# Performance work log

Hardware: AMD Instinct MI355X
Metric: run time of the kernel (lower is better)

## Reference

```python
import jax, jax.numpy as jnp
import numpy as np

H_GRU = 32  # GRU hidden size fixed to 32 in the module


def setup_inputs() -> dict:
    key = jax.random.key(0)
    ks = jax.random.split(key, 12)
    B, C_in, H, W = 64, 64, 48, 160
    C_out = 64
    s_in = 1.0 / np.sqrt(C_in)
    s_h = 1.0 / np.sqrt(H_GRU)
    u = lambda k, shape: jax.random.uniform(k, shape, jnp.float32, -s_h, s_h)
    return {
        "x": jax.random.normal(ks[0], (B, C_in, H, W), jnp.float32),
        "conv_w": jax.random.normal(ks[1], (C_out, C_in), jnp.float32) * s_in,
        "conv_b": jax.random.normal(ks[2], (C_out,), jnp.float32) * s_in,
        "wih_f": u(ks[3], (3 * H_GRU, C_out)),
        "whh_f": u(ks[4], (3 * H_GRU, H_GRU)),
        "bih_f": u(ks[5], (3 * H_GRU,)),
        "bhh_f": u(ks[6], (3 * H_GRU,)),
        "wih_b": u(ks[7], (3 * H_GRU, C_out)),
        "whh_b": u(ks[8], (3 * H_GRU, H_GRU)),
        "bih_b": u(ks[9], (3 * H_GRU,)),
        "bhh_b": u(ks[10], (3 * H_GRU,)),
    }


def _gru_scan(pre, whh, bhh):
    # pre: [N, T, 3H] input-side gate pre-activations (already x@Wih^T + bih)
    N = pre.shape[0]

    def step(h, g):
        gh = h @ whh.T + bhh
        gi_r, gi_z, gi_n = jnp.split(g, 3, axis=-1)
        gh_r, gh_z, gh_n = jnp.split(gh, 3, axis=-1)
        r = jax.nn.sigmoid(gi_r + gh_r)
        z = jax.nn.sigmoid(gi_z + gh_z)
        n = jnp.tanh(gi_n + r * gh_n)
        h_new = (1.0 - z) * n + z * h
        return h_new, h_new

    h0 = jnp.zeros((N, H_GRU), pre.dtype)
    _, ys = jax.lax.scan(step, h0, jnp.swapaxes(pre, 0, 1))  # ys: [T, N, H]
    return jnp.swapaxes(ys, 0, 1)  # [N, T, H]


def reference(x, conv_w, conv_b, wih_f, whh_f, bih_f, bhh_f,
              wih_b, whh_b, bih_b, bhh_b):
    B, C_in, H, W = x.shape
    # 1x1 conv fused with the NCHW->NHWC permute
    y = jnp.einsum('bchw,oc->bhwo', x, conv_w) + conv_b  # [B, H, W, C_out]
    C_out = y.shape[-1]
    seq = y.reshape(B * H, W, C_out)  # GRU batch = B*H, seq_len = W
    # forward direction
    pre_f = jnp.einsum('ntc,gc->ntg', seq, wih_f) + bih_f
    out_f = _gru_scan(pre_f, whh_f, bhh_f)
    # backward direction: scan reversed sequence, then flip output back
    seq_r = seq[:, ::-1, :]
    pre_b = jnp.einsum('ntc,gc->ntg', seq_r, wih_b) + bih_b
    out_b = _gru_scan(pre_b, whh_b, bhh_b)[:, ::-1, :]
    out = jnp.concatenate([out_f, out_b], axis=-1)  # [B*H, W, 2*H_GRU]
    out = out.reshape(B, H, W, 2 * H_GRU)
    return jnp.transpose(out, (0, 3, 1, 2))  # back to NCHW
```

## Files before the change

### kernel.cpp

```cpp
#include <hip/hip_runtime.h>


typedef _Float16 f16x8 __attribute__((ext_vector_type(8)));
typedef _Float16 f16x4 __attribute__((ext_vector_type(4)));
typedef __fp16   pk16  __attribute__((ext_vector_type(2)));
typedef float    f32x4 __attribute__((ext_vector_type(4)));

#define HWSTRIDE 7680
#define WS_WHH2_OFF 24576
#define WS_BIAS_OFF 36864
#define WS_X16_OFF  65536
#define NWIN 20

__global__ void fold_weights(const float* __restrict__ conv_w,
                             const float* __restrict__ conv_b,
                             const float* __restrict__ wih_f,
                             const float* __restrict__ bih_f,
                             const float* __restrict__ bhh_f,
                             const float* __restrict__ wih_b,
                             const float* __restrict__ bih_b,
                             const float* __restrict__ bhh_b,
                             const float* __restrict__ whh_f,
                             const float* __restrict__ whh_b,
                             void* wsv)
{
    _Float16* W2   = (_Float16*)wsv;
    _Float16* whh2 = (_Float16*)((char*)wsv + WS_WHH2_OFF);
    float*    bias = (float*)((char*)wsv + WS_BIAS_OFF);
    const int idx = blockIdx.x * 256 + threadIdx.x;
    if (idx < 12288) {
        const int d = idx / 6144, r = idx % 6144, g = r / 64, c = r % 64;
        const float* wih = d ? wih_b : wih_f;
        float acc = 0.f;
        for (int o = 0; o < 64; ++o) acc += wih[g * 64 + o] * conv_w[o * 64 + c];
        W2[idx] = (_Float16)acc;
    } else if (idx < 18432) {
        const int e2 = idx - 12288;
        const int dd = e2 / 3072, rr = e2 % 3072, g = rr / 32, k = rr % 32;
        const int qq = k >> 3, ee = k & 7;
        const int jsrc = (ee < 4) ? (qq * 4 + ee) : (16 + qq * 4 + (ee - 4));
        const float* whh = dd ? whh_b : whh_f;
        whh2[e2] = (_Float16)whh[g * 32 + jsrc];
    } else if (idx < 18688) {
        const int e = idx - 18432;
        const int d = e >> 7, rr = e & 127, kind = rr >> 5, j = rr & 31;
        const float* wih = d ? wih_b : wih_f;
        const float* bih = d ? bih_b : bih_f;
        const float* bhh = d ? bhh_b : bhh_f;
        float v;
        if (kind == 0 || kind == 1) {
            const int g = j + kind * 32;
            float b2 = bih[g];
            for (int o = 0; o < 64; ++o) b2 += wih[g * 64 + o] * conv_b[o];
            v = b2 + bhh[g];
        } else if (kind == 2) {
            const int g = j + 64;
            float b2 = bih[g];
            for (int o = 0; o < 64; ++o) b2 += wih[g * 64 + o] * conv_b[o];
            v = b2;
        } else {
            v = bhh[j + 64];
        }
        bias[(d * 4 + kind) * 32 + j] = v;
    }
}

static __device__ __forceinline__ unsigned pkh(float a, float b) {
    pk16 p = __builtin_amdgcn_cvt_pkrtz(a, b);
    return __builtin_bit_cast(unsigned, p);
}

__global__ __launch_bounds__(256, 2)
void xpose(const float* __restrict__ x, _Float16* __restrict__ x16)
{
    __shared__ _Float16 tile[16 * 16 * 64];
    const int bid = blockIdx.x;
    const int wc  = bid % 10;
    const int hg  = (bid / 10) % 3;
    const int b   = bid / 30;
    const int t   = threadIdx.x;
    const int s   = t >> 4;
    const int c2  = t & 15;
    const float* xb = x + (size_t)b * 64 * HWSTRIDE + (size_t)(hg * 16) * 160 + wc * 16;

    float4 pf[4][4];
    #pragma unroll
    for (int cc = 0; cc < 4; ++cc)
        #pragma unroll
        for (int k = 0; k < 4; ++k)
            pf[cc][k] = *(const float4*)(xb + (size_t)(c2 * 4 + cc) * HWSTRIDE
                                         + (size_t)s * 160 + k * 4);
    #pragma unroll
    for (int k = 0; k < 4; ++k)
        #pragma unroll
        for (int m = 0; m < 4; ++m) {
            const int w = k * 4 + m;
            uint2 v;
            v.x = pkh(((const float*)&pf[0][k])[m], ((const float*)&pf[1][k])[m]);
            v.y = pkh(((const float*)&pf[2][k])[m], ((const float*)&pf[3][k])[m]);
            const int baddr = (s * 2048 + w * 128 + c2 * 8) ^ ((s & 7) << 4);
            *(uint2*)((char*)tile + baddr) = v;
        }
    __syncthreads();
    #pragma unroll
    for (int k = 0; k < 4; ++k) {
        const int w  = k * 4 + (t >> 6);
        const int ss = (t & 63) >> 2;
        const int c0 = (t & 3) * 16;
        uint2 dv[4];
        #pragma unroll
        for (int j = 0; j < 4; ++j) {
            const int baddr = (ss * 2048 + w * 128 + c0 * 2 + j * 8) ^ ((ss & 7) << 4);
            dv[j] = *(const uint2*)((char*)tile + baddr);
        }
        _Float16* op = x16 + ((size_t)(b * 3 + hg) * 160 + wc * 16 + w) * 1024 + ss * 64 + c0;
        *(uint4*)(op)     = make_uint4(dv[0].x, dv[0].y, dv[1].x, dv[1].y);
        *(uint4*)(op + 8) = make_uint4(dv[2].x, dv[2].y, dv[3].x, dv[3].y);
    }
}

__global__ __launch_bounds__(64, 1)
void gru_fused9(const _Float16* __restrict__ x16,
                const void* __restrict__ wsv,
                float* __restrict__ out)
{
    const int bid   = blockIdx.x;
    const int d     = bid & 1;
    const int slice = bid >> 1;
    const int b     = slice / 3;
    const int hg    = slice % 3;
    const int h0    = hg * 16;
    const int lane  = threadIdx.x;
    const int q     = lane >> 4;
    const int s16   = lane & 15;

    const _Float16* W2 = (const _Float16*)wsv + (size_t)d * 96 * 64;
    f16x8 W2A[6][2];
    #pragma unroll
    for (int gt = 0; gt < 6; ++gt)
        #pragma unroll
        for (int kt = 0; kt < 2; ++kt)
            W2A[gt][kt] = *(const f16x8*)&W2[(gt * 16 + s16) * 64 + kt * 32 + q * 8];
    const _Float16* whh2 = (const _Float16*)((const char*)wsv + WS_WHH2_OFF)
                           + (size_t)d * 96 * 32;
    f16x8 whhA[6];
    #pragma unroll
    for (int gt = 0; gt < 6; ++gt)
        whhA[gt] = *(const f16x8*)&whh2[(gt * 16 + s16) * 32 + q * 8];
    const float* bias = (const float*)((const char*)wsv + WS_BIAS_OFF) + d * 128;
    float biasC[6][4];
    #pragma unroll
    for (int gt = 0; gt < 6; ++gt)
        #pragma unroll
        for (int r = 0; r < 4; ++r)
            biasC[gt][r] = bias[(gt >> 1) * 32 + (gt & 1) * 16 + 4 * q + r];
    float bhN[2][4];
    #pragma unroll
    for (int jh = 0; jh < 2; ++jh)
        #pragma unroll
        for (int r = 0; r < 4; ++r)
            bhN[jh][r] = bias[96 + jh * 16 + 4 * q + r];

    const _Float16* xsl = x16 + (size_t)slice * 160 * 1024 + s16 * 64 + q * 8;
    float* ob = out + ((size_t)b * 64 + d * 32) * HWSTRIDE + (size_t)(h0 + s16) * 160;

    f16x8 B0r[4], B1r[4];
    auto loadB = [&](int s, f16x8& B0d, f16x8& B1d) {
        const _Float16* p = xsl + (size_t)(d ? (159 - s) : s) * 1024;
        B0d = *(const f16x8*)(p);
        B1d = *(const f16x8*)(p + 32);
    };
    #pragma unroll
    for (int s0 = 0; s0 < 4; ++s0) loadB(s0, B0r[s0], B1r[s0]);

    f16x8 hB = {};
    f16x8 hB8[8];
    float hprev[8];
    #pragma unroll
    for (int uu = 0; uu < 8; ++uu) hprev[uu] = 0.f;

    #pragma unroll 1
    for (int i = 0; i < NWIN; ++i) {
        #pragma unroll
        for (int tt = 0; tt < 8; ++tt) {
            const int s = i * 8 + tt;
            f32x4 aR0 = {biasC[0][0], biasC[0][1], biasC[0][2], biasC[0][3]};
            f32x4 aR1 = {biasC[1][0], biasC[1][1], biasC[1][2], biasC[1][3]};
            f32x4 aZ0 = {biasC[2][0], biasC[2][1], biasC[2][2], biasC[2][3]};
            f32x4 aZ1 = {biasC[3][0], biasC[3][1], biasC[3][2], biasC[3][3]};
            f32x4 pN0 = {biasC[4][0], biasC[4][1], biasC[4][2], biasC[4][3]};
            f32x4 pN1 = {biasC[5][0], biasC[5][1], biasC[5][2], biasC[5][3]};
            f32x4 hN0 = {bhN[0][0], bhN[0][1], bhN[0][2], bhN[0][3]};
            f32x4 hN1 = {bhN[1][0], bhN[1][1], bhN[1][2], bhN[1][3]};
            aR0 = __builtin_amdgcn_mfma_f32_16x16x32_f16(W2A[0][0], B0r[tt & 3], aR0, 0, 0, 0);
            aR0 = __builtin_amdgcn_mfma_f32_16x16x32_f16(W2A[0][1], B1r[tt & 3], aR0, 0, 0, 0);
            aR1 = __builtin_amdgcn_mfma_f32_16x16x32_f16(W2A[1][0], B0r[tt & 3], aR1, 0, 0, 0);
            aR1 = __builtin_amdgcn_mfma_f32_16x16x32_f16(W2A[1][1], B1r[tt & 3], aR1, 0, 0, 0);
            aZ0 = __builtin_amdgcn_mfma_f32_16x16x32_f16(W2A[2][0], B0r[tt & 3], aZ0, 0, 0, 0);
            aZ0 = __builtin_amdgcn_mfma_f32_16x16x32_f16(W2A[2][1], B1r[tt & 3], aZ0, 0, 0, 0);
            aZ1 = __builtin_amdgcn_mfma_f32_16x16x32_f16(W2A[3][0], B0r[tt & 3], aZ1, 0, 0, 0);
            aZ1 = __builtin_amdgcn_mfma_f32_16x16x32_f16(W2A[3][1], B1r[tt & 3], aZ1, 0, 0, 0);
            pN0 = __builtin_amdgcn_mfma_f32_16x16x32_f16(W2A[4][0], B0r[tt & 3], pN0, 0, 0, 0);
            pN0 = __builtin_amdgcn_mfma_f32_16x16x32_f16(W2A[4][1], B1r[tt & 3], pN0, 0, 0, 0);
            pN1 = __builtin_amdgcn_mfma_f32_16x16x32_f16(W2A[5][0], B0r[tt & 3], pN1, 0, 0, 0);
            pN1 = __builtin_amdgcn_mfma_f32_16x16x32_f16(W2A[5][1], B1r[tt & 3], pN1, 0, 0, 0);
            aR0 = __builtin_amdgcn_mfma_f32_16x16x32_f16(whhA[0], hB, aR0, 0, 0, 0);
            aR1 = __builtin_amdgcn_mfma_f32_16x16x32_f16(whhA[1], hB, aR1, 0, 0, 0);
            aZ0 = __builtin_amdgcn_mfma_f32_16x16x32_f16(whhA[2], hB, aZ0, 0, 0, 0);
            aZ1 = __builtin_amdgcn_mfma_f32_16x16x32_f16(whhA[3], hB, aZ1, 0, 0, 0);
            hN0 = __builtin_amdgcn_mfma_f32_16x16x32_f16(whhA[4], hB, hN0, 0, 0, 0);
            hN1 = __builtin_amdgcn_mfma_f32_16x16x32_f16(whhA[5], hB, hN1, 0, 0, 0);
            if (tt < 4) {
                loadB(s + 4, B0r[tt & 3], B1r[tt & 3]);
            } else if (i + 1 < NWIN) {
                loadB(s + 4, B0r[tt & 3], B1r[tt & 3]);
            }
            float hn[8];
            #pragma unroll
            for (int r = 0; r < 4; ++r) {
                const float rr = __builtin_amdgcn_rcpf(1.f + __expf(-aR0[r]));
                const float zz = __builtin_amdgcn_rcpf(1.f + __expf(-aZ0[r]));
                float ta = fmaf(rr, hN0[r], pN0[r]);
                ta = fminf(fmaxf(ta, -15.f), 15.f);
                const float e2 = __expf(2.f * ta);
                const float nn = (e2 - 1.f) * __builtin_amdgcn_rcpf(e2 + 1.f);
                hn[r] = (1.f - zz) * nn + zz * hprev[r];
            }
            #pragma unroll
            for (int r = 0; r < 4; ++r) {
                const float rr = __builtin_amdgcn_rcpf(1.f + __expf(-aR1[r]));
                const float zz = __builtin_amdgcn_rcpf(1.f + __expf(-aZ1[r]));
                float ta = fmaf(rr, hN1[r], pN1[r]);
                ta = fminf(fmaxf(ta, -15.f), 15.f);
                const float e2 = __expf(2.f * ta);
                const float nn = (e2 - 1.f) * __builtin_amdgcn_rcpf(e2 + 1.f);
                hn[4 + r] = (1.f - zz) * nn + zz * hprev[4 + r];
            }
            {
                uint4 hu;
                hu.x = pkh(hn[0], hn[1]); hu.y = pkh(hn[2], hn[3]);
                hu.z = pkh(hn[4], hn[5]); hu.w = pkh(hn[6], hn[7]);
                hB = __builtin_bit_cast(f16x8, hu);
            }
            hB8[tt] = hB;
            #pragma unroll
            for (int uu = 0; uu < 8; ++uu) hprev[uu] = hn[uu];
        }
        {
            const int w0 = d ? (152 - 8 * i) : (8 * i);
            #pragma unroll
            for (int e = 0; e < 8; ++e) {
                const int j = (e >> 2) * 16 + 4 * q + (e & 3);
                float* pw = ob + (size_t)j * HWSTRIDE + w0;
                if (d == 0) {
                    *(float4*)(pw)     = make_float4((float)hB8[0][e], (float)hB8[1][e],
                                                     (float)hB8[2][e], (float)hB8[3][e]);
                    *(float4*)(pw + 4) = make_float4((float)hB8[4][e], (float)hB8[5][e],
                                                     (float)hB8[6][e], (float)hB8[7][e]);
                } else {
                    *(float4*)(pw)     = make_float4((float)hB8[7][e], (float)hB8[6][e],
                                                     (float)hB8[5][e], (float)hB8[4][e]);
                    *(float4*)(pw + 4) = make_float4((float)hB8[3][e], (float)hB8[2][e],
                                                     (float)hB8[1][e], (float)hB8[0][e]);
                }
            }
        }
    }
}

#define BAR() do { asm volatile("s_waitcnt lgkmcnt(0)" ::: "memory"); \
                   __builtin_amdgcn_s_barrier();                      \
                   asm volatile("" ::: "memory"); } while (0)

__global__ __launch_bounds__(128, 1)
void gru_fused8(const float* __restrict__ x,
                const void* __restrict__ wsv,
                float* __restrict__ out)
{
    __shared__ __align__(16) _Float16 xt[1024 * 8];
    __shared__ __align__(16) _Float16 spre[2 * 8 * 16 * 96];

    const int bid  = blockIdx.x;
    const int d    = bid / 192;
    const int g    = bid % 192;
    const int b    = g / 3;
    const int h0   = (g % 3) * 16;
    const int lane = threadIdx.x & 63;
    const int wave = threadIdx.x >> 6;
    const int sw   = bid & 1;
    const int q    = lane >> 4;
    const int s16  = lane & 15;

    const float* xb = x + (size_t)b * 64 * HWSTRIDE + (size_t)h0 * 160;

    if (wave != sw) {
        const _Float16* W2 = (const _Float16*)wsv + (size_t)d * 96 * 64;
        f16x8 W2A[6][2];
        #pragma unroll
        for (int gt = 0; gt < 6; ++gt)
            #pragma unroll
            for (int kt = 0; kt < 2; ++kt)
                W2A[gt][kt] = *(const f16x8*)&W2[(gt * 16 + s16) * 64 + kt * 32 + q * 8];
        const float* bias = (const float*)((const char*)wsv + WS_BIAS_OFF) + d * 128;
        float biasC[6][4];
        #pragma unroll
        for (int gt = 0; gt < 6; ++gt)
            #pragma unroll
            for (int r = 0; r < 4; ++r)
                biasC[gt][r] = bias[(gt >> 1) * 32 + (gt & 1) * 16 + 4 * q + r];

        float4 pf[32];
        auto load_win = [&](int wi) {
            const int w0 = d ? (152 - 8 * wi) : (8 * wi);
            #pragma unroll
            for (int k = 0; k < 16; ++k) {
                const int row = lane + 64 * k;
                const float* p = xb + (size_t)(row >> 4) * HWSTRIDE + (row & 15) * 160 + w0;
                pf[2 * k]     = *(const float4*)p;
                pf[2 * k + 1] = *(const float4*)(p + 4);
            }
        };
        auto write_xt = [&]() {
            #pragma unroll
            for (int k = 0; k < 16; ++k) {
                const int row = lane + 64 * k;
                uint4 v;
                v.x = pkh(pf[2*k].x,   pf[2*k].y);
                v.y = pkh(pf[2*k].z,   pf[2*k].w);
                v.z = pkh(pf[2*k+1].x, pf[2*k+1].y);
                v.w = pkh(pf[2*k+1].z, pf[2*k+1].w);
                *(uint4*)&xt[row * 8] = v;
            }
        };
        auto project = [&](int wi) {
            _Float16* sp = &spre[(wi & 1) * 12288];
            for (int tt = 0; tt < 8; ++tt) {
                const int wl = d ? (7 - tt) : tt;
                const int base0 = (q * 8) * 128 + s16 * 8 + wl;
                f16x8 B0, B1;
                #pragma unroll
                for (int e = 0; e < 8; ++e) {
                    B0[e] = xt[base0 + e * 128];
                    B1[e] = xt[base0 + e * 128 + 4096];
                }
                #pragma unroll
                for (int gt = 0; gt < 6; ++gt) {
                    f32x4 acc = {biasC[gt][0], biasC[gt][1], biasC[gt][2], biasC[gt][3]};
                    acc = __builtin_amdgcn_mfma_f32_16x16x32_f16(W2A[gt][0], B0, acc, 0, 0, 0);
                    acc = __builtin_amdgcn_mfma_f32_16x16x32_f16(W2A[gt][1], B1, acc, 0, 0, 0);
                    uint2 v; v.x = pkh(acc[0], acc[1]); v.y = pkh(acc[2], acc[3]);
                    const int col = (gt * 16 + 4 * q) ^ ((s16 & 7) << 2);
                    *(uint2*)&sp[(tt * 16 + s16) * 96 + col] = v;
                }
            }
        };

        load_win(0);
        #pragma unroll 1
        for (int i = 0; i < NWIN; ++i) {
            write_xt();
            project(i);
            if (i + 1 < NWIN) load_win(i + 1);
            BAR();
        }
    } else {
        const _Float16* whh2 = (const _Float16*)((const char*)wsv + WS_WHH2_OFF)
                               + (size_t)d * 96 * 32;
        f16x8 whhA[6];
        #pragma unroll
        for (int gt = 0; gt < 6; ++gt)
            whhA[gt] = *(const f16x8*)&whh2[(gt * 16 + s16) * 32 + q * 8];
        const float* bias = (const float*)((const char*)wsv + WS_BIAS_OFF) + d * 128;
        float bhN[2][4];
        #pragma unroll
        for (int jh = 0; jh < 2; ++jh)
            #pragma unroll
            for (int r = 0; r < 4; ++r)
                bhN[jh][r] = bias[96 + jh * 16 + 4 * q + r];

        float* ob = out + ((size_t)b * 64 + d * 32) * HWSTRIDE + (size_t)(h0 + s16) * 160;
        f16x8 hB = {};
        f16x8 hB8[8];
        float hprev[8];
        #pragma unroll
        for (int uu = 0; uu < 8; ++uu) hprev[uu] = 0.f;

        int spcol[6];
        #pragma unroll
        for (int gt = 0; gt < 6; ++gt)
            spcol[gt] = (gt * 16 + 4 * q) ^ ((s16 & 7) << 2);

        #pragma unroll 1
        for (int i = 0; i < NWIN; ++i) {
            BAR();
            const _Float16* sp = &spre[(i & 1) * 12288];
            f16x4 pg[4][6];
            #pragma unroll
            for (int tt = 0; tt < 8; ++tt) {
                if ((tt & 3) == 0) {
                    #pragma unroll
                    for (int t4 = 0; t4 < 4; ++t4)
                        #pragma unroll
                        for (int gt = 0; gt < 6; ++gt)
                            pg[t4][gt] = *(const f16x4*)
                                &sp[((tt + t4) * 16 + s16) * 96 + spcol[gt]];
                }
                const f16x4 p0 = pg[tt & 3][0], p1 = pg[tt & 3][1];
                const f16x4 p2 = pg[tt & 3][2], p3 = pg[tt & 3][3];
                const f16x4 p4 = pg[tt & 3][4], p5 = pg[tt & 3][5];
                f32x4 aR0 = {(float)p0[0], (float)p0[1], (float)p0[2], (float)p0[3]};
                f32x4 aR1 = {(float)p1[0], (float)p1[1], (float)p1[2], (float)p1[3]};
                f32x4 aZ0 = {(float)p2[0], (float)p2[1], (float)p2[2], (float)p2[3]};
                f32x4 aZ1 = {(float)p3[0], (float)p3[1], (float)p3[2], (float)p3[3]};
                f32x4 aN0 = {bhN[0][0], bhN[0][1], bhN[0][2], bhN[0][3]};
                f32x4 aN1 = {bhN[1][0], bhN[1][1], bhN[1][2], bhN[1][3]};
                aR0 = __builtin_amdgcn_mfma_f32_16x16x32_f16(whhA[0], hB, aR0, 0, 0, 0);
                aR1 = __builtin_amdgcn_mfma_f32_16x16x32_f16(whhA[1], hB, aR1, 0, 0, 0);
                aZ0 = __builtin_amdgcn_mfma_f32_16x16x32_f16(whhA[2], hB, aZ0, 0, 0, 0);
                aZ1 = __builtin_amdgcn_mfma_f32_16x16x32_f16(whhA[3], hB, aZ1, 0, 0, 0);
                aN0 = __builtin_amdgcn_mfma_f32_16x16x32_f16(whhA[4], hB, aN0, 0, 0, 0);
                aN1 = __builtin_amdgcn_mfma_f32_16x16x32_f16(whhA[5], hB, aN1, 0, 0, 0);
                float hn[8];
                #pragma unroll
                for (int r = 0; r < 4; ++r) {
                    const float rr = __builtin_amdgcn_rcpf(1.f + __expf(-aR0[r]));
                    const float zz = __builtin_amdgcn_rcpf(1.f + __expf(-aZ0[r]));
                    float ta = fmaf(rr, aN0[r], (float)p4[r]);
                    ta = fminf(fmaxf(ta, -15.f), 15.f);
                    const float e2 = __expf(2.f * ta);
                    const float nn = (e2 - 1.f) * __builtin_amdgcn_rcpf(e2 + 1.f);
                    hn[r] = (1.f - zz) * nn + zz * hprev[r];
                }
                #pragma unroll
                for (int r = 0; r < 4; ++r) {
                    const float rr = __builtin_amdgcn_rcpf(1.f + __expf(-aR1[r]));
                    const float zz = __builtin_amdgcn_rcpf(1.f + __expf(-aZ1[r]));
                    float ta = fmaf(rr, aN1[r], (float)p5[r]);
                    ta = fminf(fmaxf(ta, -15.f), 15.f);
                    const float e2 = __expf(2.f * ta);
                    const float nn = (e2 - 1.f) * __builtin_amdgcn_rcpf(e2 + 1.f);
                    hn[4 + r] = (1.f - zz) * nn + zz * hprev[4 + r];
                }
                {
                    uint4 hu;
                    hu.x = pkh(hn[0], hn[1]); hu.y = pkh(hn[2], hn[3]);
                    hu.z = pkh(hn[4], hn[5]); hu.w = pkh(hn[6], hn[7]);
                    hB = __builtin_bit_cast(f16x8, hu);
                }
                hB8[tt] = hB;
                #pragma unroll
                for (int uu = 0; uu < 8; ++uu) hprev[uu] = hn[uu];
            }
            {
                const int w0 = d ? (152 - 8 * i) : (8 * i);
                #pragma unroll
                for (int e = 0; e < 8; ++e) {
                    const int j = (e >> 2) * 16 + 4 * q + (e & 3);
                    float* pw = ob + (size_t)j * HWSTRIDE + w0;
                    if (d == 0) {
                        *(float4*)(pw) = make_float4((float)hB8[0][e], (float)hB8[1][e],
                                                     (float)hB8[2][e], (float)hB8[3][e]);
                        *(float4*)(pw + 4) = make_float4((float)hB8[4][e], (float)hB8[5][e],
                                                         (float)hB8[6][e], (float)hB8[7][e]);
                    } else {
                        *(float4*)(pw) = make_float4((float)hB8[7][e], (float)hB8[6][e],
                                                     (float)hB8[5][e], (float)hB8[4][e]);
                        *(float4*)(pw + 4) = make_float4((float)hB8[3][e], (float)hB8[2][e],
                                                         (float)hB8[1][e], (float)hB8[0][e]);
                    }
                }
            }
        }
    }
}

extern "C" void kernel_launch(void* const* d_in, const int* in_sizes, int n_in,
                              void* d_out, int out_size, void* d_ws, size_t ws_size,
                              hipStream_t stream) {
    (void)in_sizes; (void)n_in; (void)out_size;
    fold_weights<<<dim3(74), dim3(256), 0, stream>>>(
        (const float*)d_in[1],
        (const float*)d_in[2],
        (const float*)d_in[3],
        (const float*)d_in[5],
        (const float*)d_in[6],
        (const float*)d_in[7],
        (const float*)d_in[9],
        (const float*)d_in[10],
        (const float*)d_in[4],
        (const float*)d_in[8],
        d_ws);
    const size_t need = (size_t)WS_X16_OFF + (size_t)192 * 160 * 1024 * 2;
    if (ws_size >= need) {
        _Float16* x16 = (_Float16*)((char*)d_ws + WS_X16_OFF);
        xpose<<<dim3(1920), dim3(256), 0, stream>>>((const float*)d_in[0], x16);
        gru_fused9<<<dim3(384), dim3(64), 0, stream>>>(x16, d_ws, (float*)d_out);
    } else {
        gru_fused8<<<dim3(384), dim3(128), 0, stream>>>(
            (const float*)d_in[0], d_ws, (float*)d_out);
    }
}
```

Measured before the change: 204.6 us.

## Interleave two independent GRU slices per wavefront to hide recurrence latency

The GRU kernel now processes two H-slices per single-wave block, alternating their recurrent steps. While one step's MFMA and transcendental chain is in flight, the other slice's independent work can issue, which hides latency inside the serial recurrence. The grid shrinks from 384 to 192 blocks, so fewer CUs are busy, and each block's serial chain becomes twice as long. Loads are double-buffered with a two-step prefetch, output is written every four steps, and xpose splits its prefetch into halves so it can run at higher occupancy.

```diff
diff --git a/kernel.cpp b/kernel.cpp
--- a/kernel.cpp
+++ b/kernel.cpp
@@ -10,7 +10,6 @@
 #define WS_WHH2_OFF 24576
 #define WS_BIAS_OFF 36864
 #define WS_X16_OFF  65536
-#define NWIN 20
 
 __global__ void fold_weights(const float* __restrict__ conv_w,
                              const float* __restrict__ conv_b,
@@ -70,7 +69,7 @@
     return __builtin_bit_cast(unsigned, p);
 }
 
-__global__ __launch_bounds__(256, 2)
+__global__ __launch_bounds__(256, 4)
 void xpose(const float* __restrict__ x, _Float16* __restrict__ x16)
 {
     __shared__ _Float16 tile[16 * 16 * 64];
@@ -83,24 +82,27 @@
     const int c2  = t & 15;
     const float* xb = x + (size_t)b * 64 * HWSTRIDE + (size_t)(hg * 16) * 160 + wc * 16;
 
-    float4 pf[4][4];
     #pragma unroll
-    for (int cc = 0; cc < 4; ++cc)
-        #pragma unroll
-        for (int k = 0; k < 4; ++k)
-            pf[cc][k] = *(const float4*)(xb + (size_t)(c2 * 4 + cc) * HWSTRIDE
-                                         + (size_t)s * 160 + k * 4);
-    #pragma unroll
-    for (int k = 0; k < 4; ++k)
-        #pragma unroll
-        for (int m = 0; m < 4; ++m) {
-            const int w = k * 4 + m;
-            uint2 v;
-            v.x = pkh(((const float*)&pf[0][k])[m], ((const float*)&pf[1][k])[m]);
-            v.y = pkh(((const float*)&pf[2][k])[m], ((const float*)&pf[3][k])[m]);
-            const int baddr = (s * 2048 + w * 128 + c2 * 8) ^ ((s & 7) << 4);
-            *(uint2*)((char*)tile + baddr) = v;
-        }
+    for (int half = 0; half < 2; ++half) {
+        float4 pf[4][2];
+        #pragma unroll
+        for (int cc = 0; cc < 4; ++cc)
+            #pragma unroll
+            for (int k = 0; k < 2; ++k)
+                pf[cc][k] = *(const float4*)(xb + (size_t)(c2 * 4 + cc) * HWSTRIDE
+                                             + (size_t)s * 160 + (half * 2 + k) * 4);
+        #pragma unroll
+        for (int k = 0; k < 2; ++k)
+            #pragma unroll
+            for (int m = 0; m < 4; ++m) {
+                const int w = (half * 2 + k) * 4 + m;
+                uint2 v;
+                v.x = pkh(((const float*)&pf[0][k])[m], ((const float*)&pf[1][k])[m]);
+                v.y = pkh(((const float*)&pf[2][k])[m], ((const float*)&pf[3][k])[m]);
+                const int baddr = (s * 2048 + w * 128 + c2 * 8) ^ ((s & 7) << 4);
+                *(uint2*)((char*)tile + baddr) = v;
+            }
+    }
     __syncthreads();
     #pragma unroll
     for (int k = 0; k < 4; ++k) {
@@ -120,19 +122,16 @@
 }
 
 __global__ __launch_bounds__(64, 1)
-void gru_fused9(const _Float16* __restrict__ x16,
-                const void* __restrict__ wsv,
-                float* __restrict__ out)
+void gru_fused10(const _Float16* __restrict__ x16,
+                 const void* __restrict__ wsv,
+                 float* __restrict__ out)
 {
-    const int bid   = blockIdx.x;
-    const int d     = bid & 1;
-    const int slice = bid >> 1;
-    const int b     = slice / 3;
-    const int hg    = slice % 3;
-    const int h0    = hg * 16;
-    const int lane  = threadIdx.x;
-    const int q     = lane >> 4;
-    const int s16   = lane & 15;
+    const int bid  = blockIdx.x;
+    const int d    = bid & 1;
+    const int pr   = bid >> 1;
+    const int lane = threadIdx.x;
+    const int q    = lane >> 4;
+    const int s16  = lane & 15;
 
     const _Float16* W2 = (const _Float16*)wsv + (size_t)d * 96 * 64;
     f16x8 W2A[6][2];
@@ -161,108 +160,117 @@
         for (int r = 0; r < 4; ++r)
             bhN[jh][r] = bias[96 + jh * 16 + 4 * q + r];
 
-    const _Float16* xsl = x16 + (size_t)slice * 160 * 1024 + s16 * 64 + q * 8;
-    float* ob = out + ((size_t)b * 64 + d * 32) * HWSTRIDE + (size_t)(h0 + s16) * 160;
-
-    f16x8 B0r[4], B1r[4];
-    auto loadB = [&](int s, f16x8& B0d, f16x8& B1d) {
-        const _Float16* p = xsl + (size_t)(d ? (159 - s) : s) * 1024;
-        B0d = *(const f16x8*)(p);
-        B1d = *(const f16x8*)(p + 32);
+    const int slA = pr * 2, slB = pr * 2 + 1;
+    const _Float16* xsA = x16 + (size_t)slA * 160 * 1024 + s16 * 64 + q * 8;
+    const _Float16* xsB = x16 + (size_t)slB * 160 * 1024 + s16 * 64 + q * 8;
+    float* obA = out + ((size_t)(slA / 3) * 64 + d * 32) * HWSTRIDE
+               + (size_t)((slA % 3) * 16 + s16) * 160;
+    float* obB = out + ((size_t)(slB / 3) * 64 + d * 32) * HWSTRIDE
+               + (size_t)((slB % 3) * 16 + s16) * 160;
+
+    f16x8 rA0[2], rA1[2], rB0[2], rB1[2];
+    auto ldA = [&](int s, int slot) {
+        const _Float16* p = xsA + (size_t)(d ? (159 - s) : s) * 1024;
+        rA0[slot] = *(const f16x8*)(p);
+        rA1[slot] = *(const f16x8*)(p + 32);
     };
-    #pragma unroll
-    for (int s0 = 0; s0 < 4; ++s0) loadB(s0, B0r[s0], B1r[s0]);
-
-    f16x8 hB = {};
-    f16x8 hB8[8];
-    float hprev[8];
-    #pragma unroll
-    for (int uu = 0; uu < 8; ++uu) hprev[uu] = 0.f;
+    auto ldB = [&](int s, int slot) {
+        const _Float16* p = xsB + (size_t)(d ? (159 - s) : s) * 1024;
+        rB0[slot] = *(const f16x8*)(p);
+        rB1[slot] = *(const f16x8*)(p + 32);
+    };
+    ldA(0, 0); ldB(0, 0);
+    ldA(1, 1); ldB(1, 1);
+
+    f16x8 hA = {}, hBc = {};
+    f16x8 sbA[4], sbB[4];
+
+    auto gru_step = [&](const f16x8 B0c, const f16x8 B1c, f16x8& hc) {
+        f32x4 aR0 = {biasC[0][0], biasC[0][1], biasC[0][2], biasC[0][3]};
+        f32x4 aR1 = {biasC[1][0], biasC[1][1], biasC[1][2], biasC[1][3]};
+        f32x4 aZ0 = {biasC[2][0], biasC[2][1], biasC[2][2], biasC[2][3]};
+        f32x4 aZ1 = {biasC[3][0], biasC[3][1], biasC[3][2], biasC[3][3]};
+        f32x4 pN0 = {biasC[4][0], biasC[4][1], biasC[4][2], biasC[4][3]};
+        f32x4 pN1 = {biasC[5][0], biasC[5][1], biasC[5][2], biasC[5][3]};
+        f32x4 hN0 = {bhN[0][0], bhN[0][1], bhN[0][2], bhN[0][3]};
+        f32x4 hN1 = {bhN[1][0], bhN[1][1], bhN[1][2], bhN[1][3]};
+        aR0 = __builtin_amdgcn_mfma_f32_16x16x32_f16(W2A[0][0], B0c, aR0, 0, 0, 0);
+        aR0 = __builtin_amdgcn_mfma_f32_16x16x32_f16(W2A[0][1], B1c, aR0, 0, 0, 0);
+        aR1 = __builtin_amdgcn_mfma_f32_16x16x32_f16(W2A[1][0], B0c, aR1, 0, 0, 0);
+        aR1 = __builtin_amdgcn_mfma_f32_16x16x32_f16(W2A[1][1], B1c, aR1, 0, 0, 0);
+        aZ0 = __builtin_amdgcn_mfma_f32_16x16x32_f16(W2A[2][0], B0c, aZ0, 0, 0, 0);
+        aZ0 = __builtin_amdgcn_mfma_f32_16x16x32_f16(W2A[2][1], B1c, aZ0, 0, 0, 0);
+        aZ1 = __builtin_amdgcn_mfma_f32_16x16x32_f16(W2A[3][0], B0c, aZ1, 0, 0, 0);
+        aZ1 = __builtin_amdgcn_mfma_f32_16x16x32_f16(W2A[3][1], B1c, aZ1, 0, 0, 0);
+        pN0 = __builtin_amdgcn_mfma_f32_16x16x32_f16(W2A[4][0], B0c, pN0, 0, 0, 0);
+        pN0 = __builtin_amdgcn_mfma_f32_16x16x32_f16(W2A[4][1], B1c, pN0, 0, 0, 0);
+        pN1 = __builtin_amdgcn_mfma_f32_16x16x32_f16(W2A[5][0], B0c, pN1, 0, 0, 0);
+        pN1 = __builtin_amdgcn_mfma_f32_16x16x32_f16(W2A[5][1], B1c, pN1, 0, 0, 0);
+        aR0 = __builtin_amdgcn_mfma_f32_16x16x32_f16(whhA[0], hc, aR0, 0, 0, 0);
+        aR1 = __builtin_amdgcn_mfma_f32_16x16x32_f16(whhA[1], hc, aR1, 0, 0, 0);
+        aZ0 = __builtin_amdgcn_mfma_f32_16x16x32_f16(whhA[2], hc, aZ0, 0, 0, 0);
+        aZ1 = __builtin_amdgcn_mfma_f32_16x16x32_f16(whhA[3], hc, aZ1, 0, 0, 0);
+        hN0 = __builtin_amdgcn_mfma_f32_16x16x32_f16(whhA[4], hc, hN0, 0, 0, 0);
+        hN1 = __builtin_amdgcn_mfma_f32_16x16x32_f16(whhA[5], hc, hN1, 0, 0, 0);
+        float hn[8];
+        #pragma unroll
+        for (int r = 0; r < 4; ++r) {
+            const float rr = __builtin_amdgcn_rcpf(1.f + __expf(-aR0[r]));
+            const float zz = __builtin_amdgcn_rcpf(1.f + __expf(-aZ0[r]));
+            float ta = fmaf(rr, hN0[r], pN0[r]);
+            ta = fminf(fmaxf(ta, -15.f), 15.f);
+            const float e2 = __expf(2.f * ta);
+            const float nn = (e2 - 1.f) * __builtin_amdgcn_rcpf(e2 + 1.f);
+            hn[r] = fmaf(zz, (float)hc[r] - nn, nn);
+        }
+        #pragma unroll
+        for (int r = 0; r < 4; ++r) {
+            const float rr = __builtin_amdgcn_rcpf(1.f + __expf(-aR1[r]));
+            const float zz = __builtin_amdgcn_rcpf(1.f + __expf(-aZ1[r]));
+            float ta = fmaf(rr, hN1[r], pN1[r]);
+            ta = fminf(fmaxf(ta, -15.f), 15.f);
+            const float e2 = __expf(2.f * ta);
+            const float nn = (e2 - 1.f) * __builtin_amdgcn_rcpf(e2 + 1.f);
+            hn[4 + r] = fmaf(zz, (float)hc[4 + r] - nn, nn);
+        }
+        uint4 hu;
+        hu.x = pkh(hn[0], hn[1]); hu.y = pkh(hn[2], hn[3]);
+        hu.z = pkh(hn[4], hn[5]); hu.w = pkh(hn[6], hn[7]);
+        hc = __builtin_bit_cast(f16x8, hu);
+    };
 
     #pragma unroll 1
-    for (int i = 0; i < NWIN; ++i) {
-        #pragma unroll
-        for (int tt = 0; tt < 8; ++tt) {
-            const int s = i * 8 + tt;
-            f32x4 aR0 = {biasC[0][0], biasC[0][1], biasC[0][2], biasC[0][3]};
-            f32x4 aR1 = {biasC[1][0], biasC[1][1], biasC[1][2], biasC[1][3]};
-            f32x4 aZ0 = {biasC[2][0], biasC[2][1], biasC[2][2], biasC[2][3]};
-            f32x4 aZ1 = {biasC[3][0], biasC[3][1], biasC[3][2], biasC[3][3]};
-            f32x4 pN0 = {biasC[4][0], biasC[4][1], biasC[4][2], biasC[4][3]};
-            f32x4 pN1 = {biasC[5][0], biasC[5][1], biasC[5][2], biasC[5][3]};
-            f32x4 hN0 = {bhN[0][0], bhN[0][1], bhN[0][2], bhN[0][3]};
-            f32x4 hN1 = {bhN[1][0], bhN[1][1], bhN[1][2], bhN[1][3]};
-            aR0 = __builtin_amdgcn_mfma_f32_16x16x32_f16(W2A[0][0], B0r[tt & 3], aR0, 0, 0, 0);
-            aR0 = __builtin_amdgcn_mfma_f32_16x16x32_f16(W2A[0][1], B1r[tt & 3], aR0, 0, 0, 0);
-            aR1 = __builtin_amdgcn_mfma_f32_16x16x32_f16(W2A[1][0], B0r[tt & 3], aR1, 0, 0, 0);
-            aR1 = __builtin_amdgcn_mfma_f32_16x16x32_f16(W2A[1][1], B1r[tt & 3], aR1, 0, 0, 0);
-            aZ0 = __builtin_amdgcn_mfma_f32_16x16x32_f16(W2A[2][0], B0r[tt & 3], aZ0, 0, 0, 0);
-            aZ0 = __builtin_amdgcn_mfma_f32_16x16x32_f16(W2A[2][1], B1r[tt & 3], aZ0, 0, 0, 0);
-            aZ1 = __builtin_amdgcn_mfma_f32_16x16x32_f16(W2A[3][0], B0r[tt & 3], aZ1, 0, 0, 0);
-            aZ1 = __builtin_amdgcn_mfma_f32_16x16x32_f16(W2A[3][1], B1r[tt & 3], aZ1, 0, 0, 0);
-            pN0 = __builtin_amdgcn_mfma_f32_16x16x32_f16(W2A[4][0], B0r[tt & 3], pN0, 0, 0, 0);
-            pN0 = __builtin_amdgcn_mfma_f32_16x16x32_f16(W2A[4][1], B1r[tt & 3], pN0, 0, 0, 0);
-            pN1 = __builtin_amdgcn_mfma_f32_16x16x32_f16(W2A[5][0], B0r[tt & 3], pN1, 0, 0, 0);
-            pN1 = __builtin_amdgcn_mfma_f32_16x16x32_f16(W2A[5][1], B1r[tt & 3], pN1, 0, 0, 0);
-            aR0 = __builtin_amdgcn_mfma_f32_16x16x32_f16(whhA[0], hB, aR0, 0, 0, 0);
-            aR1 = __builtin_amdgcn_mfma_f32_16x16x32_f16(whhA[1], hB, aR1, 0, 0, 0);
-            aZ0 = __builtin_amdgcn_mfma_f32_16x16x32_f16(whhA[2], hB, aZ0, 0, 0, 0);
-            aZ1 = __builtin_amdgcn_mfma_f32_16x16x32_f16(whhA[3], hB, aZ1, 0, 0, 0);
-            hN0 = __builtin_amdgcn_mfma_f32_16x16x32_f16(whhA[4], hB, hN0, 0, 0, 0);
-            hN1 = __builtin_amdgcn_mfma_f32_16x16x32_f16(whhA[5], hB, hN1, 0, 0, 0);
-            if (tt < 4) {
-                loadB(s + 4, B0r[tt & 3], B1r[tt & 3]);
-            } else if (i + 1 < NWIN) {
-                loadB(s + 4, B0r[tt & 3], B1r[tt & 3]);
-            }
-            float hn[8];
-            #pragma unroll
-            for (int r = 0; r < 4; ++r) {
-                const float rr = __builtin_amdgcn_rcpf(1.f + __expf(-aR0[r]));
-                const float zz = __builtin_amdgcn_rcpf(1.f + __expf(-aZ0[r]));
-                float ta = fmaf(rr, hN0[r], pN0[r]);
-                ta = fminf(fmaxf(ta, -15.f), 15.f);
-                const float e2 = __expf(2.f * ta);
-                const float nn = (e2 - 1.f) * __builtin_amdgcn_rcpf(e2 + 1.f);
-                hn[r] = (1.f - zz) * nn + zz * hprev[r];
-            }
-            #pragma unroll
-            for (int r = 0; r < 4; ++r) {
-                const float rr = __builtin_amdgcn_rcpf(1.f + __expf(-aR1[r]));
-                const float zz = __builtin_amdgcn_rcpf(1.f + __expf(-aZ1[r]));
-                float ta = fmaf(rr, hN1[r], pN1[r]);
-                ta = fminf(fmaxf(ta, -15.f), 15.f);
-                const float e2 = __expf(2.f * ta);
-                const float nn = (e2 - 1.f) * __builtin_amdgcn_rcpf(e2 + 1.f);
-                hn[4 + r] = (1.f - zz) * nn + zz * hprev[4 + r];
-            }
-            {
-                uint4 hu;
-                hu.x = pkh(hn[0], hn[1]); hu.y = pkh(hn[2], hn[3]);
-                hu.z = pkh(hn[4], hn[5]); hu.w = pkh(hn[6], hn[7]);
-                hB = __builtin_bit_cast(f16x8, hu);
-            }
-            hB8[tt] = hB;
-            #pragma unroll
-            for (int uu = 0; uu < 8; ++uu) hprev[uu] = hn[uu];
-        }
-        {
-            const int w0 = d ? (152 - 8 * i) : (8 * i);
-            #pragma unroll
-            for (int e = 0; e < 8; ++e) {
-                const int j = (e >> 2) * 16 + 4 * q + (e & 3);
-                float* pw = ob + (size_t)j * HWSTRIDE + w0;
-                if (d == 0) {
-                    *(float4*)(pw)     = make_float4((float)hB8[0][e], (float)hB8[1][e],
-                                                     (float)hB8[2][e], (float)hB8[3][e]);
-                    *(float4*)(pw + 4) = make_float4((float)hB8[4][e], (float)hB8[5][e],
-                                                     (float)hB8[6][e], (float)hB8[7][e]);
-                } else {
-                    *(float4*)(pw)     = make_float4((float)hB8[7][e], (float)hB8[6][e],
-                                                     (float)hB8[5][e], (float)hB8[4][e]);
-                    *(float4*)(pw + 4) = make_float4((float)hB8[3][e], (float)hB8[2][e],
-                                                     (float)hB8[1][e], (float)hB8[0][e]);
-                }
+    for (int i = 0; i < 40; ++i) {
+        #pragma unroll
+        for (int tt = 0; tt < 4; ++tt) {
+            const int s = i * 4 + tt;
+            const int slot = s & 1;
+            const f16x8 a0 = rA0[slot], a1 = rA1[slot];
+            const f16x8 b0 = rB0[slot], b1 = rB1[slot];
+            int s2 = s + 2; if (s2 > 159) s2 = 159;
+            ldA(s2, slot);
+            ldB(s2, slot);
+            gru_step(a0, a1, hA);
+            sbA[tt] = hA;
+            gru_step(b0, b1, hBc);
+            sbB[tt] = hBc;
+        }
+        const int w0 = d ? (156 - 4 * i) : (4 * i);
+        #pragma unroll
+        for (int e = 0; e < 8; ++e) {
+            const int j = (e >> 2) * 16 + 4 * q + (e & 3);
+            float* pwA = obA + (size_t)j * HWSTRIDE + w0;
+            float* pwB = obB + (size_t)j * HWSTRIDE + w0;
+            if (d == 0) {
+                *(float4*)pwA = make_float4((float)sbA[0][e], (float)sbA[1][e],
+                                            (float)sbA[2][e], (float)sbA[3][e]);
+                *(float4*)pwB = make_float4((float)sbB[0][e], (float)sbB[1][e],
+                                            (float)sbB[2][e], (float)sbB[3][e]);
+            } else {
+                *(float4*)pwA = make_float4((float)sbA[3][e], (float)sbA[2][e],
+                                            (float)sbA[1][e], (float)sbA[0][e]);
+                *(float4*)pwB = make_float4((float)sbB[3][e], (float)sbB[2][e],
+                                            (float)sbB[1][e], (float)sbB[0][e]);
             }
         }
     }
@@ -357,10 +365,10 @@
 
         load_win(0);
         #pragma unroll 1
-        for (int i = 0; i < NWIN; ++i) {
+        for (int i = 0; i < 20; ++i) {
             write_xt();
             project(i);
-            if (i + 1 < NWIN) load_win(i + 1);
+            if (i + 1 < 20) load_win(i + 1);
             BAR();
         }
     } else {
@@ -391,7 +399,7 @@
             spcol[gt] = (gt * 16 + 4 * q) ^ ((s16 & 7) << 2);
 
         #pragma unroll 1
-        for (int i = 0; i < NWIN; ++i) {
+        for (int i = 0; i < 20; ++i) {
             BAR();
             const _Float16* sp = &spre[(i & 1) * 12288];
             f16x4 pg[4][6];
@@ -494,7 +502,7 @@
     if (ws_size >= need) {
         _Float16* x16 = (_Float16*)((char*)d_ws + WS_X16_OFF);
         xpose<<<dim3(1920), dim3(256), 0, stream>>>((const float*)d_in[0], x16);
-        gru_fused9<<<dim3(384), dim3(64), 0, stream>>>(x16, d_ws, (float*)d_out);
+        gru_fused10<<<dim3(192), dim3(64), 0, stream>>>(x16, d_ws, (float*)d_out);
     } else {
         gru_fused8<<<dim3(384), dim3(128), 0, stream>>>(
             (const float*)d_in[0], d_ws, (float*)d_out);
```

New measurement: 288.9 us. 1.41x slower.

## Split GRU hidden units across two wavefronts with per-step LDS exchange

Applied to the files above, without the earlier changes.

Replaces the single-wave GRU kernel with a two-wave version in which each wave computes half the hidden units (three gate tiles instead of six). The halves of the new hidden state are swapped through a small double-buffered shared array with a barrier every timestep. This shortens the serial per-step MFMA and transcendental chain per wave, at the cost of one block barrier and an LDS round trip on each recurrent step. It also widens output store windows to 16 steps, and splits the xpose loads into two halves with a higher occupancy hint to reduce register pressure.

```diff
diff --git a/kernel.cpp b/kernel.cpp
--- a/kernel.cpp
+++ b/kernel.cpp
@@ -2,7 +2,6 @@
 
 
 typedef _Float16 f16x8 __attribute__((ext_vector_type(8)));
-typedef _Float16 f16x4 __attribute__((ext_vector_type(4)));
 typedef __fp16   pk16  __attribute__((ext_vector_type(2)));
 typedef float    f32x4 __attribute__((ext_vector_type(4)));
 
@@ -10,7 +9,6 @@
 #define WS_WHH2_OFF 24576
 #define WS_BIAS_OFF 36864
 #define WS_X16_OFF  65536
-#define NWIN 20
 
 __global__ void fold_weights(const float* __restrict__ conv_w,
                              const float* __restrict__ conv_b,
@@ -70,7 +68,7 @@
     return __builtin_bit_cast(unsigned, p);
 }
 
-__global__ __launch_bounds__(256, 2)
+__global__ __launch_bounds__(256, 4)
 void xpose(const float* __restrict__ x, _Float16* __restrict__ x16)
 {
     __shared__ _Float16 tile[16 * 16 * 64];
@@ -83,24 +81,27 @@
     const int c2  = t & 15;
     const float* xb = x + (size_t)b * 64 * HWSTRIDE + (size_t)(hg * 16) * 160 + wc * 16;
 
-    float4 pf[4][4];
     #pragma unroll
-    for (int cc = 0; cc < 4; ++cc)
-        #pragma unroll
-        for (int k = 0; k < 4; ++k)
-            pf[cc][k] = *(const float4*)(xb + (size_t)(c2 * 4 + cc) * HWSTRIDE
-                                         + (size_t)s * 160 + k * 4);
-    #pragma unroll
-    for (int k = 0; k < 4; ++k)
-        #pragma unroll
-        for (int m = 0; m < 4; ++m) {
-            const int w = k * 4 + m;
-            uint2 v;
-            v.x = pkh(((const float*)&pf[0][k])[m], ((const float*)&pf[1][k])[m]);
-            v.y = pkh(((const float*)&pf[2][k])[m], ((const float*)&pf[3][k])[m]);
-            const int baddr = (s * 2048 + w * 128 + c2 * 8) ^ ((s & 7) << 4);
-            *(uint2*)((char*)tile + baddr) = v;
-        }
+    for (int half = 0; half < 2; ++half) {
+        float4 pf[4][2];
+        #pragma unroll
+        for (int cc = 0; cc < 4; ++cc)
+            #pragma unroll
+            for (int k = 0; k < 2; ++k)
+                pf[cc][k] = *(const float4*)(xb + (size_t)(c2 * 4 + cc) * HWSTRIDE
+                                             + (size_t)s * 160 + (half * 2 + k) * 4);
+        #pragma unroll
+        for (int k = 0; k < 2; ++k)
+            #pragma unroll
+            for (int m = 0; m < 4; ++m) {
+                const int w = (half * 2 + k) * 4 + m;
+                uint2 v;
+                v.x = pkh(((const float*)&pf[0][k])[m], ((const float*)&pf[1][k])[m]);
+                v.y = pkh(((const float*)&pf[2][k])[m], ((const float*)&pf[3][k])[m]);
+                const int baddr = (s * 2048 + w * 128 + c2 * 8) ^ ((s & 7) << 4);
+                *(uint2*)((char*)tile + baddr) = v;
+            }
+    }
     __syncthreads();
     #pragma unroll
     for (int k = 0; k < 4; ++k) {
@@ -119,158 +120,136 @@
     }
 }
 
-__global__ __launch_bounds__(64, 1)
-void gru_fused9(const _Float16* __restrict__ x16,
-                const void* __restrict__ wsv,
-                float* __restrict__ out)
+#define BARX() do { asm volatile("s_waitcnt lgkmcnt(0)" ::: "memory"); \
+                    __builtin_amdgcn_s_barrier();                      \
+                    asm volatile("" ::: "memory"); } while (0)
+
+__global__ __launch_bounds__(128, 1)
+void gru_fused11(const _Float16* __restrict__ x16,
+                 const void* __restrict__ wsv,
+                 float* __restrict__ out)
 {
+    __shared__ uint2 ex[2][2][4][16];
+
     const int bid   = blockIdx.x;
     const int d     = bid & 1;
     const int slice = bid >> 1;
     const int b     = slice / 3;
-    const int hg    = slice % 3;
-    const int h0    = hg * 16;
-    const int lane  = threadIdx.x;
+    const int h0    = (slice % 3) * 16;
+    const int lane  = threadIdx.x & 63;
+    const int jh    = threadIdx.x >> 6;
     const int q     = lane >> 4;
     const int s16   = lane & 15;
 
     const _Float16* W2 = (const _Float16*)wsv + (size_t)d * 96 * 64;
-    f16x8 W2A[6][2];
+    f16x8 W2A[3][2];
     #pragma unroll
-    for (int gt = 0; gt < 6; ++gt)
+    for (int m = 0; m < 3; ++m)
         #pragma unroll
         for (int kt = 0; kt < 2; ++kt)
-            W2A[gt][kt] = *(const f16x8*)&W2[(gt * 16 + s16) * 64 + kt * 32 + q * 8];
+            W2A[m][kt] = *(const f16x8*)&W2[((2 * m + jh) * 16 + s16) * 64 + kt * 32 + q * 8];
     const _Float16* whh2 = (const _Float16*)((const char*)wsv + WS_WHH2_OFF)
                            + (size_t)d * 96 * 32;
-    f16x8 whhA[6];
+    f16x8 whhA[3];
     #pragma unroll
-    for (int gt = 0; gt < 6; ++gt)
-        whhA[gt] = *(const f16x8*)&whh2[(gt * 16 + s16) * 32 + q * 8];
+    for (int m = 0; m < 3; ++m)
+        whhA[m] = *(const f16x8*)&whh2[((2 * m + jh) * 16 + s16) * 32 + q * 8];
+
     const float* bias = (const float*)((const char*)wsv + WS_BIAS_OFF) + d * 128;
-    float biasC[6][4];
+    const int jb = jh * 16 + 4 * q;
+    float bR[4], bZ[4], bPN[4], bHN[4];
     #pragma unroll
-    for (int gt = 0; gt < 6; ++gt)
-        #pragma unroll
-        for (int r = 0; r < 4; ++r)
-            biasC[gt][r] = bias[(gt >> 1) * 32 + (gt & 1) * 16 + 4 * q + r];
-    float bhN[2][4];
-    #pragma unroll
-    for (int jh = 0; jh < 2; ++jh)
-        #pragma unroll
-        for (int r = 0; r < 4; ++r)
-            bhN[jh][r] = bias[96 + jh * 16 + 4 * q + r];
+    for (int r = 0; r < 4; ++r) {
+        bR[r]  = bias[      jb + r];
+        bZ[r]  = bias[ 32 + jb + r];
+        bPN[r] = bias[ 64 + jb + r];
+        bHN[r] = bias[ 96 + jb + r];
+    }
 
     const _Float16* xsl = x16 + (size_t)slice * 160 * 1024 + s16 * 64 + q * 8;
     float* ob = out + ((size_t)b * 64 + d * 32) * HWSTRIDE + (size_t)(h0 + s16) * 160;
 
-    f16x8 B0r[4], B1r[4];
-    auto loadB = [&](int s, f16x8& B0d, f16x8& B1d) {
+    f16x8 rb0[4], rb1[4];
+    auto ldB = [&](int s, int slot) {
         const _Float16* p = xsl + (size_t)(d ? (159 - s) : s) * 1024;
-        B0d = *(const f16x8*)(p);
-        B1d = *(const f16x8*)(p + 32);
+        rb0[slot] = *(const f16x8*)(p);
+        rb1[slot] = *(const f16x8*)(p + 32);
     };
-    #pragma unroll
-    for (int s0 = 0; s0 < 4; ++s0) loadB(s0, B0r[s0], B1r[s0]);
+    ldB(0, 0); ldB(1, 1); ldB(2, 2); ldB(3, 3);
 
     f16x8 hB = {};
-    f16x8 hB8[8];
-    float hprev[8];
-    #pragma unroll
-    for (int uu = 0; uu < 8; ++uu) hprev[uu] = 0.f;
+    float hp[4] = {0.f, 0.f, 0.f, 0.f};
+    float hh[4][16];
 
     #pragma unroll 1
-    for (int i = 0; i < NWIN; ++i) {
-        #pragma unroll
-        for (int tt = 0; tt < 8; ++tt) {
-            const int s = i * 8 + tt;
-            f32x4 aR0 = {biasC[0][0], biasC[0][1], biasC[0][2], biasC[0][3]};
-            f32x4 aR1 = {biasC[1][0], biasC[1][1], biasC[1][2], biasC[1][3]};
-            f32x4 aZ0 = {biasC[2][0], biasC[2][1], biasC[2][2], biasC[2][3]};
-            f32x4 aZ1 = {biasC[3][0], biasC[3][1], biasC[3][2], biasC[3][3]};
-            f32x4 pN0 = {biasC[4][0], biasC[4][1], biasC[4][2], biasC[4][3]};
-            f32x4 pN1 = {biasC[5][0], biasC[5][1], biasC[5][2], biasC[5][3]};
-            f32x4 hN0 = {bhN[0][0], bhN[0][1], bhN[0][2], bhN[0][3]};
-            f32x4 hN1 = {bhN[1][0], bhN[1][1], bhN[1][2], bhN[1][3]};
-            aR0 = __builtin_amdgcn_mfma_f32_16x16x32_f16(W2A[0][0], B0r[tt & 3], aR0, 0, 0, 0);
-            aR0 = __builtin_amdgcn_mfma_f32_16x16x32_f16(W2A[0][1], B1r[tt & 3], aR0, 0, 0, 0);
-            aR1 = __builtin_amdgcn_mfma_f32_16x16x32_f16(W2A[1][0], B0r[tt & 3], aR1, 0, 0, 0);
-            aR1 = __builtin_amdgcn_mfma_f32_16x16x32_f16(W2A[1][1], B1r[tt & 3], aR1, 0, 0, 0);
-            aZ0 = __builtin_amdgcn_mfma_f32_16x16x32_f16(W2A[2][0], B0r[tt & 3], aZ0, 0, 0, 0);
-            aZ0 = __builtin_amdgcn_mfma_f32_16x16x32_f16(W2A[2][1], B1r[tt & 3], aZ0, 0, 0, 0);
-            aZ1 = __builtin_amdgcn_mfma_f32_16x16x32_f16(W2A[3][0], B0r[tt & 3], aZ1, 0, 0, 0);
-            aZ1 = __builtin_amdgcn_mfma_f32_16x16x32_f16(W2A[3][1], B1r[tt & 3], aZ1, 0, 0, 0);
-            pN0 = __builtin_amdgcn_mfma_f32_16x16x32_f16(W2A[4][0], B0r[tt & 3], pN0, 0, 0, 0);
-            pN0 = __builtin_amdgcn_mfma_f32_16x16x32_f16(W2A[4][1], B1r[tt & 3], pN0, 0, 0, 0);
-            pN1 = __builtin_amdgcn_mfma_f32_16x16x32_f16(W2A[5][0], B0r[tt & 3], pN1, 0, 0, 0);
-            pN1 = __builtin_amdgcn_mfma_f32_16x16x32_f16(W2A[5][1], B1r[tt & 3], pN1, 0, 0, 0);
-            aR0 = __builtin_amdgcn_mfma_f32_16x16x32_f16(whhA[0], hB, aR0, 0, 0, 0);
-            aR1 = __builtin_amdgcn_mfma_f32_16x16x32_f16(whhA[1], hB, aR1, 0, 0, 0);
-            aZ0 = __builtin_amdgcn_mfma_f32_16x16x32_f16(whhA[2], hB, aZ0, 0, 0, 0);
-            aZ1 = __builtin_amdgcn_mfma_f32_16x16x32_f16(whhA[3], hB, aZ1, 0, 0, 0);
-            hN0 = __builtin_amdgcn_mfma_f32_16x16x32_f16(whhA[4], hB, hN0, 0, 0, 0);
-            hN1 = __builtin_amdgcn_mfma_f32_16x16x32_f16(whhA[5], hB, hN1, 0, 0, 0);
-            if (tt < 4) {
-                loadB(s + 4, B0r[tt & 3], B1r[tt & 3]);
-            } else if (i + 1 < NWIN) {
-                loadB(s + 4, B0r[tt & 3], B1r[tt & 3]);
-            }
-            float hn[8];
+    for (int i = 0; i < 10; ++i) {
+        #pragma unroll
+        for (int tt = 0; tt < 16; ++tt) {
+            const int s = i * 16 + tt;
+            const int slot = s & 3;
+            const f16x8 b0 = rb0[slot], b1 = rb1[slot];
+            f32x4 aR  = {bR[0],  bR[1],  bR[2],  bR[3]};
+            f32x4 aZ  = {bZ[0],  bZ[1],  bZ[2],  bZ[3]};
+            f32x4 aPN = {bPN[0], bPN[1], bPN[2], bPN[3]};
+            f32x4 aHN = {bHN[0], bHN[1], bHN[2], bHN[3]};
+            aR  = __builtin_amdgcn_mfma_f32_16x16x32_f16(W2A[0][0], b0, aR,  0, 0, 0);
+            aR  = __builtin_amdgcn_mfma_f32_16x16x32_f16(W2A[0][1], b1, aR,  0, 0, 0);
+            aZ  = __builtin_amdgcn_mfma_f32_16x16x32_f16(W2A[1][0], b0, aZ,  0, 0, 0);
+            aZ  = __builtin_amdgcn_mfma_f32_16x16x32_f16(W2A[1][1], b1, aZ,  0, 0, 0);
+            aPN = __builtin_amdgcn_mfma_f32_16x16x32_f16(W2A[2][0], b0, aPN, 0, 0, 0);
+            aPN = __builtin_amdgcn_mfma_f32_16x16x32_f16(W2A[2][1], b1, aPN, 0, 0, 0);
+            aR  = __builtin_amdgcn_mfma_f32_16x16x32_f16(whhA[0], hB, aR,  0, 0, 0);
+            aZ  = __builtin_amdgcn_mfma_f32_16x16x32_f16(whhA[1], hB, aZ,  0, 0, 0);
+            aHN = __builtin_amdgcn_mfma_f32_16x16x32_f16(whhA[2], hB, aHN, 0, 0, 0);
+            {
+                int sp = s + 4; if (sp > 159) sp = 159;
+                ldB(sp, slot);
+            }
+            float hn[4];
             #pragma unroll
             for (int r = 0; r < 4; ++r) {
-                const float rr = __builtin_amdgcn_rcpf(1.f + __expf(-aR0[r]));
-                const float zz = __builtin_amdgcn_rcpf(1.f + __expf(-aZ0[r]));
-                float ta = fmaf(rr, hN0[r], pN0[r]);
+                const float rr = __builtin_amdgcn_rcpf(1.f + __expf(-aR[r]));
+                const float zz = __builtin_amdgcn_rcpf(1.f + __expf(-aZ[r]));
+                float ta = fmaf(rr, aHN[r], aPN[r]);
                 ta = fminf(fmaxf(ta, -15.f), 15.f);
                 const float e2 = __expf(2.f * ta);
                 const float nn = (e2 - 1.f) * __builtin_amdgcn_rcpf(e2 + 1.f);
-                hn[r] = (1.f - zz) * nn + zz * hprev[r];
-            }
+                hn[r] = fmaf(zz, hp[r] - nn, nn);
+                hh[r][tt] = hn[r];
+                hp[r] = hn[r];
+            }
+            uint2 own;
+            own.x = pkh(hn[0], hn[1]);
+            own.y = pkh(hn[2], hn[3]);
+            ex[s & 1][jh][q][s16] = own;
+            BARX();
+            const uint2 oth = ex[s & 1][1 - jh][q][s16];
+            uint4 hu;
+            if (jh == 0) { hu.x = own.x; hu.y = own.y; hu.z = oth.x; hu.w = oth.y; }
+            else         { hu.x = oth.x; hu.y = oth.y; hu.z = own.x; hu.w = own.y; }
+            hB = __builtin_bit_cast(f16x8, hu);
+        }
+        {
+            const int w0 = d ? (144 - 16 * i) : (16 * i);
             #pragma unroll
             for (int r = 0; r < 4; ++r) {
-                const float rr = __builtin_amdgcn_rcpf(1.f + __expf(-aR1[r]));
-                const float zz = __builtin_amdgcn_rcpf(1.f + __expf(-aZ1[r]));
-                float ta = fmaf(rr, hN1[r], pN1[r]);
-                ta = fminf(fmaxf(ta, -15.f), 15.f);
-                const float e2 = __expf(2.f * ta);
-                const float nn = (e2 - 1.f) * __builtin_amdgcn_rcpf(e2 + 1.f);
-                hn[4 + r] = (1.f - zz) * nn + zz * hprev[4 + r];
-            }
-            {
-                uint4 hu;
-                hu.x = pkh(hn[0], hn[1]); hu.y = pkh(hn[2], hn[3]);
-                hu.z = pkh(hn[4], hn[5]); hu.w = pkh(hn[6], hn[7]);
-                hB = __builtin_bit_cast(f16x8, hu);
-            }
-            hB8[tt] = hB;
-            #pragma unroll
-            for (int uu = 0; uu < 8; ++uu) hprev[uu] = hn[uu];
-        }
-        {
-            const int w0 = d ? (152 - 8 * i) : (8 * i);
-            #pragma unroll
-            for (int e = 0; e < 8; ++e) {
-                const int j = (e >> 2) * 16 + 4 * q + (e & 3);
+                const int j = jh * 16 + 4 * q + r;
                 float* pw = ob + (size_t)j * HWSTRIDE + w0;
                 if (d == 0) {
-                    *(float4*)(pw)     = make_float4((float)hB8[0][e], (float)hB8[1][e],
-                                                     (float)hB8[2][e], (float)hB8[3][e]);
-                    *(float4*)(pw + 4) = make_float4((float)hB8[4][e], (float)hB8[5][e],
-                                                     (float)hB8[6][e], (float)hB8[7][e]);
+                    #pragma unroll
+                    for (int m = 0; m < 4; ++m)
+                        *(float4*)(pw + 4 * m) =
+                            make_float4(hh[r][4*m], hh[r][4*m+1], hh[r][4*m+2], hh[r][4*m+3]);
                 } else {
-                    *(float4*)(pw)     = make_float4((float)hB8[7][e], (float)hB8[6][e],
-                                                     (float)hB8[5][e], (float)hB8[4][e]);
-                    *(float4*)(pw + 4) = make_float4((float)hB8[3][e], (float)hB8[2][e],
-                                                     (float)hB8[1][e], (float)hB8[0][e]);
-                }
-            }
-        }
-    }
-}
-
-#define BAR() do { asm volatile("s_waitcnt lgkmcnt(0)" ::: "memory"); \
-                   __builtin_amdgcn_s_barrier();                      \
-                   asm volatile("" ::: "memory"); } while (0)
+                    #pragma unroll
+                    for (int m = 0; m < 4; ++m)
+                        *(float4*)(pw + 4 * m) =
+                            make_float4(hh[r][15-4*m], hh[r][14-4*m], hh[r][13-4*m], hh[r][12-4*m]);
+                }
+            }
+        }
+    }
+}
 
 __global__ __launch_bounds__(128, 1)
 void gru_fused8(const float* __restrict__ x,
@@ -357,11 +336,11 @@
 
         load_win(0);
         #pragma unroll 1
-        for (int i = 0; i < NWIN; ++i) {
+        for (int i = 0; i < 20; ++i) {
             write_xt();
             project(i);
-            if (i + 1 < NWIN) load_win(i + 1);
-            BAR();
+            if (i + 1 < 20) load_win(i + 1);
+            BARX();
         }
     } else {
         const _Float16* whh2 = (const _Float16*)((const char*)wsv + WS_WHH2_OFF)
@@ -390,11 +369,12 @@
         for (int gt = 0; gt < 6; ++gt)
             spcol[gt] = (gt * 16 + 4 * q) ^ ((s16 & 7) << 2);
 
+        typedef _Float16 f16x4l __attribute__((ext_vector_type(4)));
         #pragma unroll 1
-        for (int i = 0; i < NWIN; ++i) {
-            BAR();
+        for (int i = 0; i < 20; ++i) {
+            BARX();
             const _Float16* sp = &spre[(i & 1) * 12288];
-            f16x4 pg[4][6];
+            f16x4l pg[4][6];
             #pragma unroll
             for (int tt = 0; tt < 8; ++tt) {
                 if ((tt & 3) == 0) {
@@ -402,12 +382,12 @@
                     for (int t4 = 0; t4 < 4; ++t4)
                         #pragma unroll
                         for (int gt = 0; gt < 6; ++gt)
-                            pg[t4][gt] = *(const f16x4*)
+                            pg[t4][gt] = *(const f16x4l*)
                                 &sp[((tt + t4) * 16 + s16) * 96 + spcol[gt]];
                 }
-                const f16x4 p0 = pg[tt & 3][0], p1 = pg[tt & 3][1];
-                const f16x4 p2 = pg[tt & 3][2], p3 = pg[tt & 3][3];
-                const f16x4 p4 = pg[tt & 3][4], p5 = pg[tt & 3][5];
+                const f16x4l p0 = pg[tt & 3][0], p1 = pg[tt & 3][1];
+                const f16x4l p2 = pg[tt & 3][2], p3 = pg[tt & 3][3];
+                const f16x4l p4 = pg[tt & 3][4], p5 = pg[tt & 3][5];
                 f32x4 aR0 = {(float)p0[0], (float)p0[1], (float)p0[2], (float)p0[3]};
                 f32x4 aR1 = {(float)p1[0], (float)p1[1], (float)p1[2], (float)p1[3]};
                 f32x4 aZ0 = {(float)p2[0], (float)p2[1], (float)p2[2], (float)p2[3]};
@@ -494,7 +474,7 @@
     if (ws_size >= need) {
         _Float16* x16 = (_Float16*)((char*)d_ws + WS_X16_OFF);
         xpose<<<dim3(1920), dim3(256), 0, stream>>>((const float*)d_in[0], x16);
-        gru_fused9<<<dim3(384), dim3(64), 0, stream>>>(x16, d_ws, (float*)d_out);
+        gru_fused11<<<dim3(384), dim3(128), 0, stream>>>(x16, d_ws, (float*)d_out);
     } else {
         gru_fused8<<<dim3(384), dim3(128), 0, stream>>>(
             (const float*)d_in[0], d_ws, (float*)d_out);
```

After: 194.5 us. 1.05x faster.
